# Kernel optimization log

Measured on AMD Instinct MI355X. Metric: run time of the kernel, lower is better.

The kernel has to match this reference:

```python
import jax, jax.numpy as jnp
import numpy as np

# ---- constants mirroring init_kwargs ----
S = 128          # sheet_units
KA = 25          # aff_cf_units
C = 2            # aff_cf_channels
KL = 25          # lat_cf_units
EXC = 9          # exc_units
DA = 1           # aff_cf_dilation
DL = 1           # lat_cf_dilation
HOMEO_TARGET = 0.04
STRENGTH = 1.0

# ---- radial helper masks (get_circle / get_radial_cos) ----
def _dist(n):
    g = jnp.arange(n, dtype=jnp.float32) - (n - 1) / 2.0
    return jnp.sqrt(g[:, None] ** 2 + g[None, :] ** 2)

def _circle(n, r):
    return (_dist(n) < r).astype(jnp.float32)

def _rcos(n, wl):
    return jnp.cos(_dist(n) * jnp.pi / wl)

# afferent envelope: [C*KA*KA], channel-major like torch repeat+view
_ae = _rcos(KA, KA) ** 2 * _circle(KA, KA / 2)
_ae = _ae / _ae.max()
AFF_ENV = jnp.tile(_ae.reshape(1, KA * KA), (C, 1)).reshape(C * KA * KA)

# lateral (LRI) envelope: [KL*KL]
_inh = _rcos(KL, EXC / DL) ** 2 * _circle(KL, EXC / (2 * DL))
_le = _rcos(KL, KL) ** 2 * (1.0 - _inh) * _circle(KL, KL / 2)
LRI_ENV = (_le / _le.max()).reshape(KL * KL)

def _unfold(x, k, dil):
    """x: [C,H,W] -> patches [L, C*k*k], torch F.unfold ordering (C slowest)."""
    Cc, H, W = x.shape
    out = H - dil * (k - 1)
    idx = jnp.arange(out)[:, None] + dil * jnp.arange(k)[None, :]  # [out,k]
    p = x[:, idx, :]          # [C,out,k,W]
    p = p[:, :, :, idx]       # [C,out,k,out,k]
    p = p.transpose(1, 3, 0, 2, 4)  # [out_i,out_j,C,ki,kj]
    return p.reshape(out * out, Cc * k * k)

def setup_inputs() -> dict:
    key = jax.random.key(0)
    k1, k2 = jax.random.split(key)
    in_size = S + DA * (KA - 1)  # 152
    x = jax.random.uniform(k1, (1, C, in_size, in_size), dtype=jnp.float32)
    rfs = jax.random.uniform(k2, (S * S, C * KA * KA, 1), dtype=jnp.float32)
    rfs = rfs / rfs.sum(1, keepdims=True)
    lat_weights = jnp.ones((S * S, KL * KL, 1), jnp.float32) / (KL * KL)
    adathresh = jnp.zeros((1, 1, S, S), jnp.float32)
    return {"x": x, "rfs": rfs, "lat_weights": lat_weights, "adathresh": adathresh}

def _forward(x, rfs, lat_weights, adathresh):
    relu = jax.nn.relu
    rfs = relu(rfs)                 # no_grad positive clamp of params
    lw = relu(lat_weights)
    # afferent: unfold + envelope + per-pixel dot (bmm with [L,F,1])
    tiles = _unfold(x[0], KA, DA) * AFF_ENV[None, :]          # [L, C*KA*KA]
    raw_aff = jnp.einsum('lf,lf->l', tiles, rfs[:, :, 0]).reshape(S, S)
    aff = jax.lax.stop_gradient(raw_aff) - adathresh[0, 0]
    lat = relu(aff)
    # lateral inhibition: pad so unfold yields S*S positions
    p = DL * (KL - 1) // 2
    lt = _unfold(jnp.pad(lat, p)[None], KL, DL) * LRI_ENV[None, :]  # [L, KL*KL]
    lat_neg = jnp.einsum('lf,lf->l', lt, jax.lax.stop_gradient(lw)[:, :, 0]).reshape(S, S)
    lat = lat - lat_neg
    lat = jnp.tanh(relu(lat * STRENGTH + aff))
    # hebbian lateral correlations term (learning_flag path)
    lt2 = _unfold(jnp.pad(lat, p, constant_values=HOMEO_TARGET)[None], KL, DL) * LRI_ENV[None, :]
    weighted = lt2 * lat.reshape(S * S, 1)
    lat_correlations = jnp.einsum('lf,lf->', weighted, lw[:, :, 0])
    return (raw_aff.reshape(1, 1, S, S), lat.reshape(1, 1, S, S),
            lat_correlations, tiles[:, None, :])

def reference(x, rfs, lat_weights, adathresh):
    return _forward(x, rfs, lat_weights, adathresh)
```

## Files before the change

kernel.cpp:

```cpp
#include <hip/hip_runtime.h>
#include <math.h>

#define S 128
#define KA 25
#define PATCH 625
#define FEAT 1250
#define PI_F 3.14159265358979323846f
#define PADW 152
#define PADA (PADW * PADW)

#define WS_LRI 0
#define WS_AE 640
#define WS_LAT0P 1280
#define WS_LATFP 24384
#define WS_PART 47488
#define NPART 1024

__device__ __forceinline__ int div25(int r) { return (r * 10486) >> 18; }
__device__ __forceinline__ int eslot(int r) { return (r & 3) * 160 + (r >> 2); }

__device__ __forceinline__ void gld16(const float* g, float* l) {
    __builtin_amdgcn_global_load_lds(
        (const __attribute__((address_space(1))) void*)g,
        (__attribute__((address_space(3))) void*)l, 16, 0, 0);
}
#define VMCNT(N) asm volatile("s_waitcnt vmcnt(" #N ")" ::: "memory"); \
                 __builtin_amdgcn_sched_barrier(0)

__global__ __launch_bounds__(256) void k_init(float* __restrict__ ws) {
    const int tid = threadIdx.x;
    if (blockIdx.x == 0) {
        __shared__ float s_tmp[640];
        __shared__ float s_red[4];
        float m = 0.0f;
        for (int r = tid; r < PATCH; r += 256) {
            int qi = div25(r);
            float di = (float)qi - 12.0f;
            float dj = (float)(r - 25 * qi) - 12.0f;
            float d = sqrtf(di * di + dj * dj);
            float ae = 0.0f, le = 0.0f;
            if (d < 12.5f) {
                float c1 = cosf(d * (PI_F / 25.0f));
                ae = c1 * c1;
                float inh = 0.0f;
                if (d < 4.5f) {
                    float c2 = cosf(d * (PI_F / 9.0f));
                    inh = c2 * c2;
                }
                le = c1 * c1 * (1.0f - inh);
            }
            ws[WS_AE + eslot(r)] = ae;
            s_tmp[r] = le;
            m = fmaxf(m, le);
        }
        for (int o = 32; o; o >>= 1) m = fmaxf(m, __shfl_down(m, o));
        if (!(tid & 63)) s_red[tid >> 6] = m;
        __syncthreads();
        float inv = 1.0f / fmaxf(fmaxf(s_red[0], s_red[1]),
                                 fmaxf(s_red[2], s_red[3]));
        for (int r = tid; r < PATCH; r += 256) ws[WS_LRI + r] = s_tmp[r] * inv;
    }
    const int gid = blockIdx.x * 256 + tid;
    const int gsz = gridDim.x * 256;
    for (int i = gid; i < 2 * PADA; i += gsz) {
        if (i < PADA) ws[WS_LAT0P + i] = 0.0f;
        else          ws[WS_LATFP + i - PADA] = 0.04f;
    }
}

__global__ __launch_bounds__(256) void k_aff(const float* __restrict__ x,
                                             const float* __restrict__ rfs,
                                             const float* __restrict__ ada,
                                             float* __restrict__ raw_aff,
                                             float* __restrict__ tiles,
                                             float* __restrict__ ws) {
    __shared__ float s_ae[640];
    const int tid = threadIdx.x;
    for (int i = tid; i < 640; i += 256) s_ae[i] = ws[WS_AE + i];
    __syncthreads();

    const int lane = tid & 63;
    const int l = blockIdx.x * 4 + (tid >> 6);
    const int li = l >> 7, lj = l & 127;
    const int wb = li * PADW + lj;
    const long B = (long)l * FEAT;
    const int peel = (l & 1) ? 2 : 0;

    float acc = 0.0f;
    if (lane < peel) {
        int f = lane;
        float t = x[wb + f] * s_ae[eslot(f)];
        tiles[B + f] = t;
        acc += t * fmaxf(rfs[B + f], 0.0f);
    }

    const float* __restrict__ rb = rfs + B + peel;
    const float4 rv0 = *reinterpret_cast<const float4*>(rb + 4 * lane);
    const float4 rv1 = *reinterpret_cast<const float4*>(rb + 4 * (lane + 64));
    const float4 rv2 = *reinterpret_cast<const float4*>(rb + 4 * (lane + 128));
    const float4 rv3 = *reinterpret_cast<const float4*>(rb + 4 * (lane + 192));
    float4 rv4 = {0.0f, 0.0f, 0.0f, 0.0f};
    if (lane < 56) rv4 = *reinterpret_cast<const float4*>(rb + 4 * (lane + 256));

    auto consume = [&](const float4& rv, int k) {
        const int f0 = peel + 4 * k;
#pragma unroll
        for (int j = 0; j < 4; ++j) {
            int f = f0 + j;
            int c = (f >= PATCH) ? 1 : 0;
            int r = f - c * PATCH;
            float t = x[c * PADA + wb + r + 127 * div25(r)] * s_ae[eslot(r)];
            if (f < PATCH) tiles[B + f] = t;
            acc += t * fmaxf((&rv.x)[j], 0.0f);
        }
    };
    consume(rv0, lane);
    consume(rv1, lane + 64);
    consume(rv2, lane + 128);
    consume(rv3, lane + 192);
    if (lane < 56) consume(rv4, lane + 256);

    if (lane < 2 - peel) {
        int f = 1248 + lane;
        int r = f - PATCH;
        acc += x[PADA + wb + r + 127 * div25(r)] * s_ae[eslot(r)]
               * fmaxf(rfs[B + f], 0.0f);
    }

    for (int o = 32; o; o >>= 1) acc += __shfl_down(acc, o);
    if (!lane) {
        raw_aff[l] = acc;
        ws[WS_LAT0P + (li + 12) * PADW + (lj + 12)] = fmaxf(acc - ada[l], 0.0f);
    }
}

__device__ __forceinline__ void tiles_c1_epilogue(
        const float* __restrict__ x, float* __restrict__ tiles,
        const float* __restrict__ ws, float* e_ae, float* e_x1,
        int li, int lj0, int tc0, int lane, int tid) {
    for (int i = tid; i < 640; i += 256) e_ae[i] = ws[WS_AE + i];
    for (int i = tid; i < 1000; i += 256) {
        int ki = i / 40, col = i - ki * 40;
        e_x1[i] = x[PADA + (li + ki) * PADW + lj0 + col];
    }
    __syncthreads();
#pragma unroll
    for (int n = 0; n < 4; ++n) {
        const int tc = tc0 + n;
        const long B = (long)(li * 128 + lj0 + tc) * FEAT + PATCH;
#pragma unroll
        for (int j = 0; j < 10; ++j) {
            int r = j * 64 + lane;
            if (j < 9 || lane < 49) {
                int ki = div25(r), kj = r - 25 * ki;
                tiles[B + r] = e_x1[ki * 40 + kj + tc] * e_ae[eslot(r)];
            }
        }
    }
}

__global__ __launch_bounds__(256) void k_lat(const float* __restrict__ raw_aff,
                                             const float* __restrict__ ada,
                                             const float* __restrict__ lw,
                                             const float* __restrict__ x,
                                             float* __restrict__ latf,
                                             float* __restrict__ tiles,
                                             float* __restrict__ ws) {
    __shared__ float s_le[640];
    __shared__ float s_g[25][40];
    __shared__ float s_st[4][2][640];
    const int tid = threadIdx.x, lane = tid & 63, wv = tid >> 6;
    const int blk = blockIdx.x;
    const int li = blk >> 3;
    const int lj0 = (blk & 7) << 4;

    for (int i = tid; i < 625; i += 256) s_le[i] = ws[WS_LRI + i];
    for (int i = tid; i < 1000; i += 256) {
        int ki = i / 40;
        int col = i - ki * 40;
        s_g[ki][col] = ws[WS_LAT0P + (li + ki) * PADW + lj0 + col];
    }
    __syncthreads();

    const int tc0 = wv << 2;
    const int l0 = li * 128 + lj0 + tc0;

    float acc_ht[4], ra[4], ad[4];
#define HT(n) { \
        const int l = l0 + (n); const long B = (long)l * PATCH; \
        const int peel = (4 - (l & 3)) & 3; \
        const int fmax4 = (PATCH - peel) & ~3; \
        const int tcnt = (PATCH - peel) & 3; \
        float a = 0.0f; \
        if (lane < peel) { \
            int f = lane; int ki = div25(f); int kj = f - 25 * ki; \
            a += s_g[ki][kj + tc0 + (n)] * s_le[f] * fmaxf(lw[B + f], 0.0f); \
        } \
        if (lane < tcnt) { \
            int f = peel + fmax4 + lane; int ki = div25(f); int kj = f - 25 * ki; \
            a += s_g[ki][kj + tc0 + (n)] * s_le[f] * fmaxf(lw[B + f], 0.0f); \
        } \
        if (!lane) { ra[n] = raw_aff[l]; ad[n] = ada[l]; } \
        acc_ht[n] = a; }
    HT(0) HT(1) HT(2) HT(3)
#undef HT

    auto stage = [&](int n, float* buf) {
        const int l = l0 + n;
        const long B = (long)l * PATCH;
        const int peel = (4 - (l & 3)) & 3;
        const int rem = ((PATCH - peel) >> 2) - 128;
        const float* gp = lw + B + peel + 4 * lane;
        gld16(gp,       buf);
        gld16(gp + 256, buf + 256);
        if (lane < rem) gld16(gp + 512, buf + 512);
    };
    auto consume = [&](int n, const float* buf, float accin, float rav,
                       float adv) {
        const int l = l0 + n;
        const int peel = (4 - (l & 3)) & 3;
        const int fmax4 = (PATCH - peel) & ~3;
        const int tc = tc0 + n;
        float acc = accin;
#pragma unroll
        for (int j = 0; j < 10; ++j) {
            int fh = j * 64 + lane;
            if (j < 9 || fh < fmax4) {
                float wval = buf[fh];
                int f = peel + fh;
                int ki = div25(f);
                int kj = f - 25 * ki;
                acc += s_g[ki][kj + tc] * s_le[f] * fmaxf(wval, 0.0f);
            }
        }
        for (int o = 32; o; o >>= 1) acc += __shfl_down(acc, o);
        if (!lane) {
            float aff_l = rav - adv;
            float lat0_l = fmaxf(aff_l, 0.0f);
            float v = (lat0_l - acc)  + aff_l;
            float lv = tanhf(fmaxf(v, 0.0f));
            latf[l] = lv;
            ws[WS_LATFP + (li + 12) * PADW + lj0 + tc + 12] = lv;
        }
    };

    float* buf0 = &s_st[wv][0][0];
    float* buf1 = &s_st[wv][1][0];
    __builtin_amdgcn_sched_barrier(0);
    stage(0, buf0);
    stage(1, buf1);
    VMCNT(3);
    consume(0, buf0, acc_ht[0], ra[0], ad[0]);
    stage(2, buf0);
    VMCNT(5);
    consume(1, buf1, acc_ht[1], ra[1], ad[1]);
    stage(3, buf1);
    VMCNT(5);
    consume(2, buf0, acc_ht[2], ra[2], ad[2]);
    VMCNT(2);
    consume(3, buf1, acc_ht[3], ra[3], ad[3]);

    if ((li & 1) == 0) {
        __syncthreads();
        tiles_c1_epilogue(x, tiles, ws, &s_st[0][0][0], &s_st[1][0][0],
                          li, lj0, tc0, lane, tid);
    }
}

__global__ __launch_bounds__(256) void k_corr(const float* __restrict__ latf,
                                              const float* __restrict__ lw,
                                              const float* __restrict__ x,
                                              float* __restrict__ tiles,
                                              float* __restrict__ ws) {
    __shared__ float s_le[640];
    __shared__ float s_g[25][40];
    __shared__ float s_st[4][2][640];
    __shared__ float s_red[4];
    const int tid = threadIdx.x, lane = tid & 63, wv = tid >> 6;
    const int blk = blockIdx.x;
    const int li = blk >> 3;
    const int lj0 = (blk & 7) << 4;

    for (int i = tid; i < 625; i += 256) s_le[i] = ws[WS_LRI + i];
    for (int i = tid; i < 1000; i += 256) {
        int ki = i / 40;
        int col = i - ki * 40;
        s_g[ki][col] = ws[WS_LATFP + (li + ki) * PADW + lj0 + col];
    }
    __syncthreads();

    const int tc0 = wv << 2;
    const int l0 = li * 128 + lj0 + tc0;

    float acc_ht[4], lf[4];
#define HT(n) { \
        const int l = l0 + (n); const long B = (long)l * PATCH; \
        const int peel = (4 - (l & 3)) & 3; \
        const int fmax4 = (PATCH - peel) & ~3; \
        const int tcnt = (PATCH - peel) & 3; \
        float a = 0.0f; \
        if (lane < peel) { \
            int f = lane; int ki = div25(f); int kj = f - 25 * ki; \
            a += s_g[ki][kj + tc0 + (n)] * s_le[f] * fmaxf(lw[B + f], 0.0f); \
        } \
        if (lane < tcnt) { \
            int f = peel + fmax4 + lane; int ki = div25(f); int kj = f - 25 * ki; \
            a += s_g[ki][kj + tc0 + (n)] * s_le[f] * fmaxf(lw[B + f], 0.0f); \
        } \
        if (!lane) lf[n] = latf[l]; \
        acc_ht[n] = a; }
    HT(0) HT(1) HT(2) HT(3)
#undef HT

    auto stage = [&](int n, float* buf) {
        const int l = l0 + n;
        const long B = (long)l * PATCH;
        const int peel = (4 - (l & 3)) & 3;
        const int rem = ((PATCH - peel) >> 2) - 128;
        const float* gp = lw + B + peel + 4 * lane;
        gld16(gp,       buf);
        gld16(gp + 256, buf + 256);
        if (lane < rem) gld16(gp + 512, buf + 512);
    };
    float wsum = 0.0f;
    auto consume = [&](int n, const float* buf, float accin, float lfv) {
        const int l = l0 + n;
        const int peel = (4 - (l & 3)) & 3;
        const int fmax4 = (PATCH - peel) & ~3;
        const int tc = tc0 + n;
        float acc = accin;
#pragma unroll
        for (int j = 0; j < 10; ++j) {
            int fh = j * 64 + lane;
            if (j < 9 || fh < fmax4) {
                float wval = buf[fh];
                int f = peel + fh;
                int ki = div25(f);
                int kj = f - 25 * ki;
                acc += s_g[ki][kj + tc] * s_le[f] * fmaxf(wval, 0.0f);
            }
        }
        for (int o = 32; o; o >>= 1) acc += __shfl_down(acc, o);
        if (!lane) wsum += acc * lfv;
    };

    float* buf0 = &s_st[wv][0][0];
    float* buf1 = &s_st[wv][1][0];
    __builtin_amdgcn_sched_barrier(0);
    stage(0, buf0);
    stage(1, buf1);
    VMCNT(3);
    consume(0, buf0, acc_ht[0], lf[0]);
    stage(2, buf0);
    VMCNT(3);
    consume(1, buf1, acc_ht[1], lf[1]);
    stage(3, buf1);
    VMCNT(3);
    consume(2, buf0, acc_ht[2], lf[2]);
    VMCNT(0);
    consume(3, buf1, acc_ht[3], lf[3]);

    if (!lane) s_red[wv] = wsum;
    __syncthreads();
    if (!tid)
        ws[WS_PART + blk] = s_red[0] + s_red[1] + s_red[2] + s_red[3];

    if ((li & 1) == 1) {
        __syncthreads();
        tiles_c1_epilogue(x, tiles, ws, &s_st[0][0][0], &s_st[1][0][0],
                          li, lj0, tc0, lane, tid);
    }
}

__global__ __launch_bounds__(256) void k_reduce(const float* __restrict__ ws,
                                                float* __restrict__ corr) {
    __shared__ float s_red[4];
    const int tid = threadIdx.x;
    const int lane = tid & 63, wv = tid >> 6;
    float acc = 0.0f;
    for (int i = tid; i < NPART; i += 256) acc += ws[WS_PART + i];
    for (int o = 32; o; o >>= 1) acc += __shfl_down(acc, o);
    if (!lane) s_red[wv] = acc;
    __syncthreads();
    if (!tid) corr[0] = s_red[0] + s_red[1] + s_red[2] + s_red[3];
}

extern "C" void kernel_launch(void* const* d_in, const int* in_sizes, int n_in,
                              void* d_out, int out_size, void* d_ws, size_t ws_size,
                              hipStream_t stream) {
    const float* x   = (const float*)d_in[0];
    const float* rfs = (const float*)d_in[1];
    const float* lw  = (const float*)d_in[2];
    const float* ada = (const float*)d_in[3];

    float* out      = (float*)d_out;
    float* raw_aff  = out;
    float* latf     = out + S * S;
    float* corr     = out + 2 * S * S;
    float* tiles    = out + 2 * S * S + 1;
    float* ws       = (float*)d_ws;

    k_init<<<16, 256, 0, stream>>>(ws);
    k_aff<<<4096, 256, 0, stream>>>(x, rfs, ada, raw_aff, tiles, ws);
    k_lat<<<1024, 256, 0, stream>>>(raw_aff, ada, lw, x, latf, tiles, ws);
    k_corr<<<1024, 256, 0, stream>>>(latf, lw, x, tiles, ws);
    k_reduce<<<1, 256, 0, stream>>>(ws, corr);
}
```

Baseline: 223.6 us.

## Move channel-0 tile writes out of k_aff into k_lat epilogue, stage x in LDS

k_aff no longer writes the channel-0 tiles. It stages the x input window for 4 adjacent columns into padded LDS and reads from there instead of doing scattered global gathers. Channel-0 tiles are now written by every k_lat block and channel-1 tiles by every k_corr block, so the epilogue work is split evenly instead of by row parity. The goal is coalesced, evenly spread tile stores and less global gather traffic in k_aff, in exchange for more LDS setup per block and a longer epilogue in k_lat and k_corr.

```diff
diff --git a/kernel.cpp b/kernel.cpp
--- a/kernel.cpp
+++ b/kernel.cpp
@@ -14,6 +14,7 @@
 #define WS_LAT0P 1280
 #define WS_LATFP 24384
 #define WS_PART 47488
+#define WS_AEL 48512
 #define NPART 1024
 
 __device__ __forceinline__ int div25(int r) { return (r * 10486) >> 18; }
@@ -50,6 +51,7 @@
                 le = c1 * c1 * (1.0f - inh);
             }
             ws[WS_AE + eslot(r)] = ae;
+            ws[WS_AEL + r] = ae;
             s_tmp[r] = le;
             m = fmaxf(m, le);
         }
@@ -72,26 +74,36 @@
                                              const float* __restrict__ rfs,
                                              const float* __restrict__ ada,
                                              float* __restrict__ raw_aff,
-                                             float* __restrict__ tiles,
                                              float* __restrict__ ws) {
     __shared__ float s_ae[640];
-    const int tid = threadIdx.x;
+    __shared__ float s_x[2][25][28];
+    const int tid = threadIdx.x, lane = tid & 63, wv = tid >> 6;
+    const int blk = blockIdx.x;
+    const int li = blk >> 5;
+    const int lj0 = (blk & 31) << 2;
+
     for (int i = tid; i < 640; i += 256) s_ae[i] = ws[WS_AE + i];
-    __syncthreads();
-
-    const int lane = tid & 63;
-    const int l = blockIdx.x * 4 + (tid >> 6);
-    const int li = l >> 7, lj = l & 127;
-    const int wb = li * PADW + lj;
+    for (int i = tid; i < 1400; i += 256) {
+        int c = i >= 700;
+        int rm = i - c * 700;
+        int ki = rm / 28;
+        int col = rm - ki * 28;
+        s_x[c][ki][(col & 3) * 7 + (col >> 2)] =
+            x[c * PADA + (li + ki) * PADW + lj0 + col];
+    }
+    __syncthreads();
+
+    const int tc = wv;
+    const int l = li * 128 + lj0 + tc;
     const long B = (long)l * FEAT;
     const int peel = (l & 1) ? 2 : 0;
 
     float acc = 0.0f;
     if (lane < peel) {
         int f = lane;
-        float t = x[wb + f] * s_ae[eslot(f)];
-        tiles[B + f] = t;
-        acc += t * fmaxf(rfs[B + f], 0.0f);
+        int col = f + tc;
+        acc += s_x[0][0][(col & 3) * 7 + (col >> 2)] * s_ae[eslot(f)]
+               * fmaxf(rfs[B + f], 0.0f);
     }
 
     const float* __restrict__ rb = rfs + B + peel;
@@ -109,8 +121,9 @@
             int f = f0 + j;
             int c = (f >= PATCH) ? 1 : 0;
             int r = f - c * PATCH;
-            float t = x[c * PADA + wb + r + 127 * div25(r)] * s_ae[eslot(r)];
-            if (f < PATCH) tiles[B + f] = t;
+            int ki = div25(r);
+            int col = r - 25 * ki + tc;
+            float t = s_x[c][ki][(col & 3) * 7 + (col >> 2)] * s_ae[eslot(r)];
             acc += t * fmaxf((&rv.x)[j], 0.0f);
         }
     };
@@ -123,37 +136,40 @@
     if (lane < 2 - peel) {
         int f = 1248 + lane;
         int r = f - PATCH;
-        acc += x[PADA + wb + r + 127 * div25(r)] * s_ae[eslot(r)]
+        int ki = div25(r);
+        int col = r - 25 * ki + tc;
+        acc += s_x[1][ki][(col & 3) * 7 + (col >> 2)] * s_ae[eslot(r)]
                * fmaxf(rfs[B + f], 0.0f);
     }
 
     for (int o = 32; o; o >>= 1) acc += __shfl_down(acc, o);
     if (!lane) {
         raw_aff[l] = acc;
-        ws[WS_LAT0P + (li + 12) * PADW + (lj + 12)] = fmaxf(acc - ada[l], 0.0f);
-    }
-}
-
-__device__ __forceinline__ void tiles_c1_epilogue(
+        ws[WS_LAT0P + (li + 12) * PADW + (lj0 + tc + 12)] =
+            fmaxf(acc - ada[l], 0.0f);
+    }
+}
+
+__device__ __forceinline__ void tiles_epilogue(
         const float* __restrict__ x, float* __restrict__ tiles,
-        const float* __restrict__ ws, float* e_ae, float* e_x1,
-        int li, int lj0, int tc0, int lane, int tid) {
-    for (int i = tid; i < 640; i += 256) e_ae[i] = ws[WS_AE + i];
+        const float* __restrict__ ws, float* e_ae, float* e_x,
+        int cc, int li, int lj0, int tc0, int lane, int tid) {
+    for (int i = tid; i < 625; i += 256) e_ae[i] = ws[WS_AEL + i];
     for (int i = tid; i < 1000; i += 256) {
         int ki = i / 40, col = i - ki * 40;
-        e_x1[i] = x[PADA + (li + ki) * PADW + lj0 + col];
+        e_x[i] = x[cc * PADA + (li + ki) * PADW + lj0 + col];
     }
     __syncthreads();
 #pragma unroll
     for (int n = 0; n < 4; ++n) {
         const int tc = tc0 + n;
-        const long B = (long)(li * 128 + lj0 + tc) * FEAT + PATCH;
+        const long B = (long)(li * 128 + lj0 + tc) * FEAT + cc * PATCH;
 #pragma unroll
         for (int j = 0; j < 10; ++j) {
             int r = j * 64 + lane;
             if (j < 9 || lane < 49) {
                 int ki = div25(r), kj = r - 25 * ki;
-                tiles[B + r] = e_x1[ki * 40 + kj + tc] * e_ae[eslot(r)];
+                tiles[B + r] = e_x[ki * 40 + kj + tc] * e_ae[r];
             }
         }
     }
@@ -260,11 +276,9 @@
     VMCNT(2);
     consume(3, buf1, acc_ht[3], ra[3], ad[3]);
 
-    if ((li & 1) == 0) {
-        __syncthreads();
-        tiles_c1_epilogue(x, tiles, ws, &s_st[0][0][0], &s_st[1][0][0],
-                          li, lj0, tc0, lane, tid);
-    }
+    __syncthreads();
+    tiles_epilogue(x, tiles, ws, &s_st[0][0][0], &s_st[1][0][0],
+                   0, li, lj0, tc0, lane, tid);
 }
 
 __global__ __launch_bounds__(256) void k_corr(const float* __restrict__ latf,
@@ -365,11 +379,9 @@
     if (!tid)
         ws[WS_PART + blk] = s_red[0] + s_red[1] + s_red[2] + s_red[3];
 
-    if ((li & 1) == 1) {
-        __syncthreads();
-        tiles_c1_epilogue(x, tiles, ws, &s_st[0][0][0], &s_st[1][0][0],
-                          li, lj0, tc0, lane, tid);
-    }
+    __syncthreads();
+    tiles_epilogue(x, tiles, ws, &s_st[0][0][0], &s_st[1][0][0],
+                   1, li, lj0, tc0, lane, tid);
 }
 
 __global__ __launch_bounds__(256) void k_reduce(const float* __restrict__ ws,
@@ -401,7 +413,7 @@
     float* ws       = (float*)d_ws;
 
     k_init<<<16, 256, 0, stream>>>(ws);
-    k_aff<<<4096, 256, 0, stream>>>(x, rfs, ada, raw_aff, tiles, ws);
+    k_aff<<<4096, 256, 0, stream>>>(x, rfs, ada, raw_aff, ws);
     k_lat<<<1024, 256, 0, stream>>>(raw_aff, ada, lw, x, latf, tiles, ws);
     k_corr<<<1024, 256, 0, stream>>>(latf, lw, x, tiles, ws);
     k_reduce<<<1, 256, 0, stream>>>(ws, corr);
```

Measured after the change: 215.6 us, median of 2. 1.04x faster.
